# Performance work log

Measured on AMD Instinct MI355X. Metric: run time of the kernel, lower is better.

## Reference

```python
import jax, jax.numpy as jnp
import numpy as np

TOP_K = 2  # config.top_k


def setup_inputs() -> dict:
    key = jax.random.key(0)
    k0, k1, k2, k3, k4 = jax.random.split(key, 5)
    B, S, D, F, E = 1, 2048, 512, 1024, 8
    scale = 0.02
    hidden_states = jax.random.normal(k0, (B, S, D), dtype=jnp.float32)
    router_w = jax.random.normal(k1, (D, E), dtype=jnp.float32) * scale
    w1 = jax.random.normal(k2, (E, D, F), dtype=jnp.float32) * scale  # gate proj
    w2 = jax.random.normal(k3, (E, F, D), dtype=jnp.float32) * scale  # down proj
    w3 = jax.random.normal(k4, (E, D, F), dtype=jnp.float32) * scale  # up proj
    return {"hidden_states": hidden_states, "router_w": router_w,
            "w1": w1, "w2": w2, "w3": w3}


def reference(hidden_states, router_w, w1, w2, w3):
    B, S, D = hidden_states.shape
    E = router_w.shape[1]
    x = hidden_states.reshape(-1, D)                      # [T, D]
    T = x.shape[0]

    # router: softmax in float32, top-k, renormalize (matches torch source)
    router_logits = x @ router_w                          # [T, E]
    probs = jax.nn.softmax(router_logits.astype(jnp.float32), axis=-1)
    routing_weights, selected_experts = jax.lax.top_k(probs, TOP_K)  # [T, K]
    routing_weights = routing_weights / routing_weights.sum(axis=-1, keepdims=True)
    routing_weights = routing_weights.astype(x.dtype)

    # combine weights: scatter top-k weights into dense [T, E] (one-hot combine)
    combine = jnp.zeros((T, E), dtype=x.dtype).at[
        jnp.arange(T)[:, None], selected_experts].add(routing_weights)

    # dense-all-experts evaluation, math-identical to gather-GEMM-scatter:
    # unselected experts get combine weight 0 and contribute nothing.
    gate = jax.nn.silu(jnp.einsum('td,edf->tef', x, w1))  # [T, E, F]
    up = jnp.einsum('td,edf->tef', x, w3)                 # [T, E, F]
    h = gate * up * combine[:, :, None]                   # weight before down-proj
    out = jnp.einsum('tef,efd->td', h, w2)                # [T, D]
    return out.reshape(B, S, D)
```

## Files before the change

kernel.cpp:

```cpp
#include <hip/hip_runtime.h>
#include <hip/hip_bf16.h>


typedef __attribute__((ext_vector_type(4))) float f32x4;
typedef __attribute__((ext_vector_type(8))) __bf16 bf16x8;

#define T_TOK 2048
#define DMODEL 512
#define FFN 1024
#define NE 8
#define MAXMB 40
#define PCAP (MAXMB * 128)

__device__ __forceinline__ void gload_lds16(const void* g, void* l) {
  __builtin_amdgcn_global_load_lds(
      (const __attribute__((address_space(1))) void*)g,
      (__attribute__((address_space(3))) void*)l, 16, 0, 0);
}

#define PIPE_BAR_8()                                        \
  asm volatile("s_waitcnt vmcnt(8)" ::: "memory");          \
  __builtin_amdgcn_s_barrier();                             \
  __builtin_amdgcn_sched_barrier(0)
#define PIPE_BAR_6()                                        \
  asm volatile("s_waitcnt vmcnt(6)" ::: "memory");          \
  __builtin_amdgcn_s_barrier();                             \
  __builtin_amdgcn_sched_barrier(0)
#define PIPE_BAR_0()                                        \
  asm volatile("s_waitcnt vmcnt(0)" ::: "memory");          \
  __builtin_amdgcn_s_barrier();                             \
  __builtin_amdgcn_sched_barrier(0)
#define POST_BAR()                                          \
  __builtin_amdgcn_s_barrier();                             \
  __builtin_amdgcn_sched_barrier(0)

__global__ __launch_bounds__(256) void prep_kernel(
    const float* __restrict__ x, const float* __restrict__ rw,
    const float* __restrict__ w1, const float* __restrict__ w2,
    const float* __restrict__ w3, __bf16* __restrict__ xb,
    __bf16* __restrict__ w1t, __bf16* __restrict__ w2t,
    __bf16* __restrict__ w3t, int* __restrict__ tope, float* __restrict__ topw,
    int* __restrict__ pair_t, float* __restrict__ pair_w,
    int* __restrict__ sched_e) {
  __shared__ __bf16 tile[64][65];
  const int bx = blockIdx.x;
  const int tid = threadIdx.x;

  if (bx < 3072) {
    const float* src;
    __bf16* dst;
    int R, C, idx;
    if (bx < 1024)      { src = w1; dst = w1t; R = 512;  C = 1024; idx = bx; }
    else if (bx < 2048) { src = w3; dst = w3t; R = 512;  C = 1024; idx = bx - 1024; }
    else                { src = w2; dst = w2t; R = 1024; C = 512;  idx = bx - 2048; }
    const int ntx = C >> 6, nty = R >> 6;
    const int cx = idx % ntx;
    const int gry = idx / ntx;
    const int e = gry / nty;
    const int r0 = (gry % nty) * 64;
    const int c0 = cx * 64;
    src += (size_t)e * R * C;
    dst += (size_t)e * R * C;
#pragma unroll
    for (int q = 0; q < 4; ++q) {
      const int r = (tid >> 4) + q * 16;
      const int c = (tid & 15) * 4;
      const f32x4 v = *(const f32x4*)&src[(size_t)(r0 + r) * C + c0 + c];
      tile[r][c] = (__bf16)v[0];
      tile[r][c + 1] = (__bf16)v[1];
      tile[r][c + 2] = (__bf16)v[2];
      tile[r][c + 3] = (__bf16)v[3];
    }
    __syncthreads();
#pragma unroll
    for (int p = 0; p < 2; ++p) {
      const int cc = (tid >> 3) + p * 32;
      const int rr = (tid & 7) * 8;
      union { bf16x8 v; __bf16 s[8]; } u;
#pragma unroll
      for (int i = 0; i < 8; ++i) u.s[i] = tile[rr + i][cc];
      *(bf16x8*)&dst[(size_t)(c0 + cc) * R + r0 + rr] = u.v;
    }
  } else if (bx < 3584) {
    const int t = (bx - 3072) * 4 + (tid >> 6);
    const int lane = tid & 63;
    const float* xr = x + (size_t)t * DMODEL + lane * 8;
    const f32x4 a = *(const f32x4*)xr;
    const f32x4 b = *(const f32x4*)(xr + 4);
    bf16x8 v;
    v[0] = (__bf16)a[0]; v[1] = (__bf16)a[1]; v[2] = (__bf16)a[2]; v[3] = (__bf16)a[3];
    v[4] = (__bf16)b[0]; v[5] = (__bf16)b[1]; v[6] = (__bf16)b[2]; v[7] = (__bf16)b[3];
    *(bf16x8*)&xb[(size_t)t * DMODEL + lane * 8] = v;

    float xv[8] = {a[0], a[1], a[2], a[3], b[0], b[1], b[2], b[3]};
    float part[NE];
#pragma unroll
    for (int e = 0; e < NE; ++e) part[e] = 0.f;
#pragma unroll
    for (int i = 0; i < 8; ++i) {
      const int d = lane * 8 + i;
      const f32x4 r0 = *(const f32x4*)&rw[(size_t)d * NE];
      const f32x4 r1 = *(const f32x4*)&rw[(size_t)d * NE + 4];
      part[0] += xv[i] * r0[0]; part[1] += xv[i] * r0[1];
      part[2] += xv[i] * r0[2]; part[3] += xv[i] * r0[3];
      part[4] += xv[i] * r1[0]; part[5] += xv[i] * r1[1];
      part[6] += xv[i] * r1[2]; part[7] += xv[i] * r1[3];
    }
#pragma unroll
    for (int off = 32; off > 0; off >>= 1) {
#pragma unroll
      for (int e = 0; e < NE; ++e) part[e] += __shfl_xor(part[e], off);
    }
    if (lane == 0) {
      int ia = 0;
#pragma unroll
      for (int e = 1; e < NE; ++e)
        if (part[e] > part[ia]) ia = e;
      int ib = (ia == 0) ? 1 : 0;
#pragma unroll
      for (int e = 0; e < NE; ++e)
        if (e != ia && e != ib && part[e] > part[ib]) ib = e;
      const float wa = 1.f / (1.f + __expf(part[ib] - part[ia]));
      tope[t * 2] = ia;
      tope[t * 2 + 1] = ib;
      topw[t * 2] = wa;
      topw[t * 2 + 1] = 1.f - wa;
    }
  } else {
    const int i = (bx - 3584) * 256 + tid;
    for (int j = i; j < PCAP; j += 2048) { pair_t[j] = 0; pair_w[j] = 0.f; }
    if (i < MAXMB) sched_e[i] = -1;
  }
}

__global__ __launch_bounds__(256) void build_kernel(
    const int* __restrict__ tope, const float* __restrict__ topw,
    int* __restrict__ pair_t, float* __restrict__ pair_w,
    int* __restrict__ pairidx, int* __restrict__ sched_e) {
  __shared__ int cnt[NE], base[NE], ofs[NE];
  const int tid = threadIdx.x;
  if (tid < NE) { cnt[tid] = 0; ofs[tid] = 0; }
  __syncthreads();
  for (int t = tid; t < T_TOK; t += 256) {
    atomicAdd(&cnt[tope[t * 2]], 1);
    atomicAdd(&cnt[tope[t * 2 + 1]], 1);
  }
  __syncthreads();
  if (tid == 0) {
    int mb = 0;
    for (int e = 0; e < NE; ++e) {
      base[e] = mb * 128;
      const int nmb = (cnt[e] + 127) >> 7;
      for (int i = 0; i < nmb; ++i) sched_e[mb + i] = e;
      mb += nmb;
    }
  }
  __syncthreads();
  for (int t = tid; t < T_TOK; t += 256) {
#pragma unroll
    for (int s = 0; s < 2; ++s) {
      const int e = tope[t * 2 + s];
      const int pos = base[e] + atomicAdd(&ofs[e], 1);
      pair_t[pos] = t;
      pair_w[pos] = topw[t * 2 + s];
      pairidx[t * 2 + s] = pos;
    }
  }
}

__global__ __launch_bounds__(256) void gemm1_kernel(
    const __bf16* __restrict__ xb, const __bf16* __restrict__ w1t,
    const __bf16* __restrict__ w3t, const int* __restrict__ pair_t,
    const float* __restrict__ pair_w, const int* __restrict__ sched_e,
    __bf16* __restrict__ hbuf) {
  __shared__ alignas(16) __bf16 As[2][128 * 64];
  __shared__ alignas(16) __bf16 B1s[2][64 * 64];
  __shared__ alignas(16) __bf16 B3s[2][64 * 64];
  __shared__ float comb[128];
  const int tid = threadIdx.x;
  const int id = blockIdx.x;
  const int mb = (id & 7) + ((id >> 7) << 3);
  const int f0 = ((id >> 3) & 15) * 64;
  const int e = sched_e[mb];
  if (e < 0) return;
  const int m0 = mb * 128;
  const int lane = tid & 63;
  const int wv = tid >> 6;
  const int wr = wv >> 1, wc = wv & 1;
  const int l15 = lane & 15, lhi = lane >> 4;
  const int sw = (l15 & 7) << 4;

  if (tid < 128) comb[tid] = pair_w[m0 + tid];

  size_t aoff[4];
  int lbA[4];
#pragma unroll
  for (int it = 0; it < 4; ++it) {
    const int chunk = it * 256 + tid;
    const int r = chunk >> 3;
    const int c8 = ((chunk & 7) ^ (r & 7)) * 8;
    aoff[it] = (size_t)pair_t[m0 + r] * DMODEL + c8;
    lbA[it] = (it * 256 + (tid & ~63)) * 16;
  }
  size_t boff[2];
  int lbB[2];
#pragma unroll
  for (int it = 0; it < 2; ++it) {
    const int chunk = it * 256 + tid;
    const int r = chunk >> 3;
    const int c8 = ((chunk & 7) ^ (r & 7)) * 8;
    boff[it] = (size_t)(e * FFN + f0 + r) * DMODEL + c8;
    lbB[it] = (it * 256 + (tid & ~63)) * 16;
  }

  const f32x4 fz = {0.f, 0.f, 0.f, 0.f};
  f32x4 acc1[4][2], acc3[4][2];
#pragma unroll
  for (int m = 0; m < 4; ++m)
#pragma unroll
    for (int n = 0; n < 2; ++n) { acc1[m][n] = fz; acc3[m][n] = fz; }

#define G1_STAGE(BUF, K0)                                                     \
  do {                                                                        \
    _Pragma("unroll") for (int it = 0; it < 4; ++it)                          \
        gload_lds16(xb + aoff[it] + (K0), (char*)As[BUF] + lbA[it]);          \
    _Pragma("unroll") for (int it = 0; it < 2; ++it) {                        \
      gload_lds16(w1t + boff[it] + (K0), (char*)B1s[BUF] + lbB[it]);          \
      gload_lds16(w3t + boff[it] + (K0), (char*)B3s[BUF] + lbB[it]);          \
    }                                                                         \
  } while (0)

#define G1_COMPUTE(BUF)                                                       \
  do {                                                                        \
    __builtin_amdgcn_s_setprio(1);                                            \
    _Pragma("unroll") for (int kk = 0; kk < 2; ++kk) {                        \
      const int ko = (kk * 64 + lhi * 16) ^ sw;                               \
      bf16x8 af[4], b1f[2], b3f[2];                                           \
      _Pragma("unroll") for (int m = 0; m < 4; ++m)                           \
          af[m] = *(const bf16x8*)((const char*)As[BUF] +                     \
                                   (wr * 64 + m * 16 + l15) * 128 + ko);      \
      _Pragma("unroll") for (int n = 0; n < 2; ++n) {                         \
        const int ro = (wc * 32 + n * 16 + l15) * 128 + ko;                   \
        b1f[n] = *(const bf16x8*)((const char*)B1s[BUF] + ro);                \
        b3f[n] = *(const bf16x8*)((const char*)B3s[BUF] + ro);                \
      }                                                                       \
      _Pragma("unroll") for (int m = 0; m < 4; ++m)                           \
          _Pragma("unroll") for (int n = 0; n < 2; ++n) {                     \
        acc1[m][n] = __builtin_amdgcn_mfma_f32_16x16x32_bf16(af[m], b1f[n],   \
                                                             acc1[m][n], 0, 0, 0); \
        acc3[m][n] = __builtin_amdgcn_mfma_f32_16x16x32_bf16(af[m], b3f[n],   \
                                                             acc3[m][n], 0, 0, 0); \
      }                                                                       \
    }                                                                         \
    __builtin_amdgcn_s_setprio(0);                                            \
  } while (0)

  G1_STAGE(0, 0);
#pragma unroll
  for (int t = 0; t < 7; ++t) {
    G1_STAGE((t + 1) & 1, (t + 1) * 64);
    PIPE_BAR_8();
    G1_COMPUTE(t & 1);
    POST_BAR();
  }
  PIPE_BAR_0();
  G1_COMPUTE(1);

  __syncthreads();
  {
    __bf16* eps = (__bf16*)As;
    constexpr int EW = 72;
#pragma unroll
    for (int m = 0; m < 4; ++m)
#pragma unroll
      for (int n = 0; n < 2; ++n)
#pragma unroll
        for (int r = 0; r < 4; ++r) {
          const int row = wr * 64 + m * 16 + lhi * 4 + r;
          const int col = wc * 32 + n * 16 + l15;
          const float g = acc1[m][n][r];
          const float u = acc3[m][n][r];
          eps[row * EW + col] = (__bf16)((g / (1.f + __expf(-g))) * u * comb[row]);
        }
    __syncthreads();
#pragma unroll
    for (int p = 0; p < 4; ++p) {
      const int i = p * 256 + tid;
      const int row = i >> 3, c8 = (i & 7) * 8;
      *(bf16x8*)&hbuf[(size_t)(m0 + row) * FFN + f0 + c8] =
          *(const bf16x8*)&eps[row * EW + c8];
    }
  }
#undef G1_STAGE
#undef G1_COMPUTE
}

__global__ __launch_bounds__(256) void gemm2_kernel(
    const __bf16* __restrict__ hbuf, const __bf16* __restrict__ w2t,
    const int* __restrict__ sched_e, __bf16* __restrict__ outp) {
  __shared__ alignas(16) __bf16 As[2][128 * 64];
  __shared__ alignas(16) __bf16 Bs[2][64 * 64];
  const int tid = threadIdx.x;
  const int id = blockIdx.x;
  const int gk = (id & 7) + ((id >> 6) << 3);
  const int n0 = ((id >> 3) & 7) * 64;
  const int mb = gk >> 1;
  const int kz = gk & 1;
  const int e = sched_e[mb];
  if (e < 0) return;
  const int m0 = mb * 128;
  const int fbase = kz * (FFN / 2);
  const int lane = tid & 63;
  const int wv = tid >> 6;
  const int wr = wv >> 1, wc = wv & 1;
  const int l15 = lane & 15, lhi = lane >> 4;
  const int sw = (l15 & 7) << 4;

  size_t aoff[4];
  int lbA[4];
#pragma unroll
  for (int it = 0; it < 4; ++it) {
    const int chunk = it * 256 + tid;
    const int r = chunk >> 3;
    const int c8 = ((chunk & 7) ^ (r & 7)) * 8;
    aoff[it] = (size_t)(m0 + r) * FFN + fbase + c8;
    lbA[it] = (it * 256 + (tid & ~63)) * 16;
  }
  size_t boff[2];
  int lbB[2];
#pragma unroll
  for (int it = 0; it < 2; ++it) {
    const int chunk = it * 256 + tid;
    const int r = chunk >> 3;
    const int c8 = ((chunk & 7) ^ (r & 7)) * 8;
    boff[it] = ((size_t)e * DMODEL + n0 + r) * FFN + fbase + c8;
    lbB[it] = (it * 256 + (tid & ~63)) * 16;
  }

  const f32x4 fz = {0.f, 0.f, 0.f, 0.f};
  f32x4 acc[4][2];
#pragma unroll
  for (int m = 0; m < 4; ++m) { acc[m][0] = fz; acc[m][1] = fz; }

#define G2_STAGE(BUF, K0)                                                     \
  do {                                                                        \
    _Pragma("unroll") for (int it = 0; it < 4; ++it)                          \
        gload_lds16(hbuf + aoff[it] + (K0), (char*)As[BUF] + lbA[it]);        \
    _Pragma("unroll") for (int it = 0; it < 2; ++it)                          \
        gload_lds16(w2t + boff[it] + (K0), (char*)Bs[BUF] + lbB[it]);         \
  } while (0)

#define G2_COMPUTE(BUF)                                                       \
  do {                                                                        \
    __builtin_amdgcn_s_setprio(1);                                            \
    _Pragma("unroll") for (int kk = 0; kk < 2; ++kk) {                        \
      const int ko = (kk * 64 + lhi * 16) ^ sw;                               \
      bf16x8 af[4], bfr[2];                                                   \
      _Pragma("unroll") for (int m = 0; m < 4; ++m)                           \
          af[m] = *(const bf16x8*)((const char*)As[BUF] +                     \
                                   (wr * 64 + m * 16 + l15) * 128 + ko);      \
      _Pragma("unroll") for (int n = 0; n < 2; ++n)                           \
          bfr[n] = *(const bf16x8*)((const char*)Bs[BUF] +                    \
                                    (wc * 32 + n * 16 + l15) * 128 + ko);     \
      _Pragma("unroll") for (int m = 0; m < 4; ++m)                           \
          _Pragma("unroll") for (int n = 0; n < 2; ++n)                       \
              acc[m][n] = __builtin_amdgcn_mfma_f32_16x16x32_bf16(            \
                  af[m], bfr[n], acc[m][n], 0, 0, 0);                         \
    }                                                                         \
    __builtin_amdgcn_s_setprio(0);                                            \
  } while (0)

  G2_STAGE(0, 0);
#pragma unroll
  for (int t = 0; t < 7; ++t) {
    G2_STAGE((t + 1) & 1, (t + 1) * 64);
    PIPE_BAR_6();
    G2_COMPUTE(t & 1);
    POST_BAR();
  }
  PIPE_BAR_0();
  G2_COMPUTE(1);

  __syncthreads();
  {
    __bf16* eps = (__bf16*)As;
    constexpr int EW = 72;
#pragma unroll
    for (int m = 0; m < 4; ++m)
#pragma unroll
      for (int n = 0; n < 2; ++n)
#pragma unroll
        for (int r = 0; r < 4; ++r) {
          const int row = wr * 64 + m * 16 + lhi * 4 + r;
          const int col = wc * 32 + n * 16 + l15;
          eps[row * EW + col] = (__bf16)acc[m][n][r];
        }
    __syncthreads();
#pragma unroll
    for (int p = 0; p < 4; ++p) {
      const int i = p * 256 + tid;
      const int row = i >> 3, c8 = (i & 7) * 8;
      *(bf16x8*)&outp[((size_t)kz * PCAP + m0 + row) * DMODEL + n0 + c8] =
          *(const bf16x8*)&eps[row * EW + c8];
    }
  }
#undef G2_STAGE
#undef G2_COMPUTE
}

__global__ __launch_bounds__(256) void gather_kernel(
    const __bf16* __restrict__ outp, const int* __restrict__ pairidx,
    float* __restrict__ out) {
  const int i = blockIdx.x * 256 + threadIdx.x;
  const int t = i >> 6;
  const int c = (i & 63) * 8;
  const int p0 = pairidx[t * 2];
  const int p1 = pairidx[t * 2 + 1];
  const size_t KZ = (size_t)PCAP * DMODEL;
  const bf16x8 a0 = *(const bf16x8*)&outp[(size_t)p0 * DMODEL + c];
  const bf16x8 a1 = *(const bf16x8*)&outp[(size_t)p1 * DMODEL + c];
  const bf16x8 b0 = *(const bf16x8*)&outp[KZ + (size_t)p0 * DMODEL + c];
  const bf16x8 b1 = *(const bf16x8*)&outp[KZ + (size_t)p1 * DMODEL + c];
  f32x4 lo, hi;
#pragma unroll
  for (int j = 0; j < 4; ++j)
    lo[j] = (float)a0[j] + (float)a1[j] + (float)b0[j] + (float)b1[j];
#pragma unroll
  for (int j = 0; j < 4; ++j)
    hi[j] = (float)a0[j + 4] + (float)a1[j + 4] + (float)b0[j + 4] + (float)b1[j + 4];
  float* op = out + (size_t)t * DMODEL + c;
  *(f32x4*)op = lo;
  *(f32x4*)(op + 4) = hi;
}

extern "C" void kernel_launch(void* const* d_in, const int* in_sizes, int n_in,
                              void* d_out, int out_size, void* d_ws, size_t ws_size,
                              hipStream_t stream) {
  const float* x = (const float*)d_in[0];
  const float* rw = (const float*)d_in[1];
  const float* w1 = (const float*)d_in[2];
  const float* w2 = (const float*)d_in[3];
  const float* w3 = (const float*)d_in[4];
  float* out = (float*)d_out;
  char* ws = (char*)d_ws;

  int* tope = (int*)(ws + 0);
  float* topw = (float*)(ws + 16384);
  int* pair_t = (int*)(ws + 32768);
  float* pair_w = (float*)(ws + 53248);
  int* pairidx = (int*)(ws + 73728);
  int* sched_e = (int*)(ws + 90112);
  __bf16* xb = (__bf16*)(ws + 98304);
  __bf16* w1t = (__bf16*)(ws + 2195456);
  __bf16* w3t = (__bf16*)(ws + 10584064);
  __bf16* w2t = (__bf16*)(ws + 18972672);
  __bf16* hbuf = (__bf16*)(ws + 27361280);
  __bf16* outp = (__bf16*)(ws + 37847040);

  hipLaunchKernelGGL(prep_kernel, dim3(3592), dim3(256), 0, stream,
                     x, rw, w1, w2, w3, xb, w1t, w2t, w3t, tope, topw,
                     pair_t, pair_w, sched_e);
  hipLaunchKernelGGL(build_kernel, dim3(1), dim3(256), 0, stream,
                     tope, topw, pair_t, pair_w, pairidx, sched_e);
  hipLaunchKernelGGL(gemm1_kernel, dim3(640), dim3(256), 0, stream,
                     xb, w1t, w3t, pair_t, pair_w, sched_e, hbuf);
  hipLaunchKernelGGL(gemm2_kernel, dim3(640), dim3(256), 0, stream,
                     hbuf, w2t, sched_e, outp);
  hipLaunchKernelGGL(gather_kernel, dim3(512), dim3(256), 0, stream,
                     outp, pairidx, out);
}
```

Baseline: 72.90 us.

## Fuse weight fp32-to-bf16 transpose into GEMM B-tile staging

Removes the separate weight transpose/convert pass from the prep kernel. The GEMM kernels now load fp32 weights straight into registers, convert them to bf16 and write them transposed and swizzled into LDS. This avoids writing and re-reading the bf16 weight copies (about 24 MB of extra traffic). In exchange, each M-block re-reads the fp32 weights, which are twice as wide, and the pipeline is reworked so that each stage waits on vmcnt(0) before the register-to-LDS write, which may reduce overlap.

```diff
diff --git a/kernel.cpp b/kernel.cpp
--- a/kernel.cpp
+++ b/kernel.cpp
@@ -4,6 +4,7 @@
 
 typedef __attribute__((ext_vector_type(4))) float f32x4;
 typedef __attribute__((ext_vector_type(8))) __bf16 bf16x8;
+typedef __attribute__((ext_vector_type(2))) __bf16 bf16x2;
 
 #define T_TOK 2048
 #define DMODEL 512
@@ -18,71 +19,23 @@
       (__attribute__((address_space(3))) void*)l, 16, 0, 0);
 }
 
-#define PIPE_BAR_8()                                        \
-  asm volatile("s_waitcnt vmcnt(8)" ::: "memory");          \
+#define VM0()                                               \
+  asm volatile("s_waitcnt vmcnt(0)" ::: "memory");          \
+  __builtin_amdgcn_sched_barrier(0)
+#define LG0_BAR()                                           \
+  asm volatile("s_waitcnt lgkmcnt(0)" ::: "memory");        \
   __builtin_amdgcn_s_barrier();                             \
   __builtin_amdgcn_sched_barrier(0)
-#define PIPE_BAR_6()                                        \
-  asm volatile("s_waitcnt vmcnt(6)" ::: "memory");          \
-  __builtin_amdgcn_s_barrier();                             \
-  __builtin_amdgcn_sched_barrier(0)
-#define PIPE_BAR_0()                                        \
-  asm volatile("s_waitcnt vmcnt(0)" ::: "memory");          \
-  __builtin_amdgcn_s_barrier();                             \
-  __builtin_amdgcn_sched_barrier(0)
-#define POST_BAR()                                          \
-  __builtin_amdgcn_s_barrier();                             \
-  __builtin_amdgcn_sched_barrier(0)
 
 __global__ __launch_bounds__(256) void prep_kernel(
     const float* __restrict__ x, const float* __restrict__ rw,
-    const float* __restrict__ w1, const float* __restrict__ w2,
-    const float* __restrict__ w3, __bf16* __restrict__ xb,
-    __bf16* __restrict__ w1t, __bf16* __restrict__ w2t,
-    __bf16* __restrict__ w3t, int* __restrict__ tope, float* __restrict__ topw,
+    __bf16* __restrict__ xb, int* __restrict__ tope, float* __restrict__ topw,
     int* __restrict__ pair_t, float* __restrict__ pair_w,
     int* __restrict__ sched_e) {
-  __shared__ __bf16 tile[64][65];
   const int bx = blockIdx.x;
   const int tid = threadIdx.x;
-
-  if (bx < 3072) {
-    const float* src;
-    __bf16* dst;
-    int R, C, idx;
-    if (bx < 1024)      { src = w1; dst = w1t; R = 512;  C = 1024; idx = bx; }
-    else if (bx < 2048) { src = w3; dst = w3t; R = 512;  C = 1024; idx = bx - 1024; }
-    else                { src = w2; dst = w2t; R = 1024; C = 512;  idx = bx - 2048; }
-    const int ntx = C >> 6, nty = R >> 6;
-    const int cx = idx % ntx;
-    const int gry = idx / ntx;
-    const int e = gry / nty;
-    const int r0 = (gry % nty) * 64;
-    const int c0 = cx * 64;
-    src += (size_t)e * R * C;
-    dst += (size_t)e * R * C;
-#pragma unroll
-    for (int q = 0; q < 4; ++q) {
-      const int r = (tid >> 4) + q * 16;
-      const int c = (tid & 15) * 4;
-      const f32x4 v = *(const f32x4*)&src[(size_t)(r0 + r) * C + c0 + c];
-      tile[r][c] = (__bf16)v[0];
-      tile[r][c + 1] = (__bf16)v[1];
-      tile[r][c + 2] = (__bf16)v[2];
-      tile[r][c + 3] = (__bf16)v[3];
-    }
-    __syncthreads();
-#pragma unroll
-    for (int p = 0; p < 2; ++p) {
-      const int cc = (tid >> 3) + p * 32;
-      const int rr = (tid & 7) * 8;
-      union { bf16x8 v; __bf16 s[8]; } u;
-#pragma unroll
-      for (int i = 0; i < 8; ++i) u.s[i] = tile[rr + i][cc];
-      *(bf16x8*)&dst[(size_t)(c0 + cc) * R + r0 + rr] = u.v;
-    }
-  } else if (bx < 3584) {
-    const int t = (bx - 3072) * 4 + (tid >> 6);
+  if (bx < 512) {
+    const int t = bx * 4 + (tid >> 6);
     const int lane = tid & 63;
     const float* xr = x + (size_t)t * DMODEL + lane * 8;
     const f32x4 a = *(const f32x4*)xr;
@@ -127,7 +80,7 @@
       topw[t * 2 + 1] = 1.f - wa;
     }
   } else {
-    const int i = (bx - 3584) * 256 + tid;
+    const int i = (bx - 512) * 256 + tid;
     for (int j = i; j < PCAP; j += 2048) { pair_t[j] = 0; pair_w[j] = 0.f; }
     if (i < MAXMB) sched_e[i] = -1;
   }
@@ -169,8 +122,8 @@
 }
 
 __global__ __launch_bounds__(256) void gemm1_kernel(
-    const __bf16* __restrict__ xb, const __bf16* __restrict__ w1t,
-    const __bf16* __restrict__ w3t, const int* __restrict__ pair_t,
+    const __bf16* __restrict__ xb, const float* __restrict__ w1,
+    const float* __restrict__ w3, const int* __restrict__ pair_t,
     const float* __restrict__ pair_w, const int* __restrict__ sched_e,
     __bf16* __restrict__ hbuf) {
   __shared__ alignas(16) __bf16 As[2][128 * 64];
@@ -189,6 +142,7 @@
   const int wr = wv >> 1, wc = wv & 1;
   const int l15 = lane & 15, lhi = lane >> 4;
   const int sw = (l15 & 7) << 4;
+  const int dp = tid & 31, fq = tid >> 5;
 
   if (tid < 128) comb[tid] = pair_w[m0 + tid];
 
@@ -202,16 +156,8 @@
     aoff[it] = (size_t)pair_t[m0 + r] * DMODEL + c8;
     lbA[it] = (it * 256 + (tid & ~63)) * 16;
   }
-  size_t boff[2];
-  int lbB[2];
-#pragma unroll
-  for (int it = 0; it < 2; ++it) {
-    const int chunk = it * 256 + tid;
-    const int r = chunk >> 3;
-    const int c8 = ((chunk & 7) ^ (r & 7)) * 8;
-    boff[it] = (size_t)(e * FFN + f0 + r) * DMODEL + c8;
-    lbB[it] = (it * 256 + (tid & ~63)) * 16;
-  }
+  const float* b1base = w1 + ((size_t)e * DMODEL + 2 * dp) * FFN + f0 + fq * 8;
+  const float* b3base = w3 + ((size_t)e * DMODEL + 2 * dp) * FFN + f0 + fq * 8;
 
   const f32x4 fz = {0.f, 0.f, 0.f, 0.f};
   f32x4 acc1[4][2], acc3[4][2];
@@ -220,13 +166,36 @@
 #pragma unroll
     for (int n = 0; n < 2; ++n) { acc1[m][n] = fz; acc3[m][n] = fz; }
 
-#define G1_STAGE(BUF, K0)                                                     \
+  f32x4 q1[4], q3[4];
+
+#define G1_LOADB(K0)                                                          \
+  do {                                                                        \
+    const float* p1 = b1base + (size_t)(K0)*FFN;                              \
+    const float* p3 = b3base + (size_t)(K0)*FFN;                              \
+    q1[0] = *(const f32x4*)p1;        q1[1] = *(const f32x4*)(p1 + 4);        \
+    q1[2] = *(const f32x4*)(p1 + FFN); q1[3] = *(const f32x4*)(p1 + FFN + 4); \
+    q3[0] = *(const f32x4*)p3;        q3[1] = *(const f32x4*)(p3 + 4);        \
+    q3[2] = *(const f32x4*)(p3 + FFN); q3[3] = *(const f32x4*)(p3 + FFN + 4); \
+  } while (0)
+
+#define G1_STAGEA(BUF, K0)                                                    \
   do {                                                                        \
     _Pragma("unroll") for (int it = 0; it < 4; ++it)                          \
         gload_lds16(xb + aoff[it] + (K0), (char*)As[BUF] + lbA[it]);          \
-    _Pragma("unroll") for (int it = 0; it < 2; ++it) {                        \
-      gload_lds16(w1t + boff[it] + (K0), (char*)B1s[BUF] + lbB[it]);          \
-      gload_lds16(w3t + boff[it] + (K0), (char*)B3s[BUF] + lbB[it]);          \
+  } while (0)
+
+#define G1_WRITEB(BUF)                                                        \
+  do {                                                                        \
+    _Pragma("unroll") for (int fi = 0; fi < 8; ++fi) {                        \
+      const float l1 = fi < 4 ? q1[0][fi] : q1[1][fi - 4];                    \
+      const float h1 = fi < 4 ? q1[2][fi] : q1[3][fi - 4];                    \
+      const float l3 = fi < 4 ? q3[0][fi] : q3[1][fi - 4];                    \
+      const float h3 = fi < 4 ? q3[2][fi] : q3[3][fi - 4];                    \
+      const int ad = (fq * 8 + fi) * 128 + ((dp * 4) ^ (fi << 4));            \
+      bf16x2 v1 = {(__bf16)l1, (__bf16)h1};                                   \
+      bf16x2 v3 = {(__bf16)l3, (__bf16)h3};                                   \
+      *(bf16x2*)((char*)B1s[BUF] + ad) = v1;                                  \
+      *(bf16x2*)((char*)B3s[BUF] + ad) = v3;                                  \
     }                                                                         \
   } while (0)
 
@@ -255,15 +224,20 @@
     __builtin_amdgcn_s_setprio(0);                                            \
   } while (0)
 
-  G1_STAGE(0, 0);
+  G1_LOADB(0);
+  G1_STAGEA(0, 0);
+  VM0();
+  G1_WRITEB(0);
+  LG0_BAR();
 #pragma unroll
   for (int t = 0; t < 7; ++t) {
-    G1_STAGE((t + 1) & 1, (t + 1) * 64);
-    PIPE_BAR_8();
+    G1_LOADB((t + 1) * 64);
+    G1_STAGEA((t + 1) & 1, (t + 1) * 64);
     G1_COMPUTE(t & 1);
-    POST_BAR();
-  }
-  PIPE_BAR_0();
+    VM0();
+    G1_WRITEB((t + 1) & 1);
+    LG0_BAR();
+  }
   G1_COMPUTE(1);
 
   __syncthreads();
@@ -291,12 +265,14 @@
           *(const bf16x8*)&eps[row * EW + c8];
     }
   }
-#undef G1_STAGE
+#undef G1_LOADB
+#undef G1_STAGEA
+#undef G1_WRITEB
 #undef G1_COMPUTE
 }
 
 __global__ __launch_bounds__(256) void gemm2_kernel(
-    const __bf16* __restrict__ hbuf, const __bf16* __restrict__ w2t,
+    const __bf16* __restrict__ hbuf, const float* __restrict__ w2,
     const int* __restrict__ sched_e, __bf16* __restrict__ outp) {
   __shared__ alignas(16) __bf16 As[2][128 * 64];
   __shared__ alignas(16) __bf16 Bs[2][64 * 64];
@@ -315,6 +291,7 @@
   const int wr = wv >> 1, wc = wv & 1;
   const int l15 = lane & 15, lhi = lane >> 4;
   const int sw = (l15 & 7) << 4;
+  const int fp = tid & 31, dq = tid >> 5;
 
   size_t aoff[4];
   int lbA[4];
@@ -326,28 +303,37 @@
     aoff[it] = (size_t)(m0 + r) * FFN + fbase + c8;
     lbA[it] = (it * 256 + (tid & ~63)) * 16;
   }
-  size_t boff[2];
-  int lbB[2];
-#pragma unroll
-  for (int it = 0; it < 2; ++it) {
-    const int chunk = it * 256 + tid;
-    const int r = chunk >> 3;
-    const int c8 = ((chunk & 7) ^ (r & 7)) * 8;
-    boff[it] = ((size_t)e * DMODEL + n0 + r) * FFN + fbase + c8;
-    lbB[it] = (it * 256 + (tid & ~63)) * 16;
-  }
+  const float* bbase = w2 + ((size_t)e * FFN + fbase + 2 * fp) * DMODEL + n0 + dq * 8;
 
   const f32x4 fz = {0.f, 0.f, 0.f, 0.f};
   f32x4 acc[4][2];
 #pragma unroll
   for (int m = 0; m < 4; ++m) { acc[m][0] = fz; acc[m][1] = fz; }
 
-#define G2_STAGE(BUF, K0)                                                     \
+  f32x4 q[4];
+
+#define G2_LOADB(K0)                                                          \
+  do {                                                                        \
+    const float* p = bbase + (size_t)(K0)*DMODEL;                             \
+    q[0] = *(const f32x4*)p;            q[1] = *(const f32x4*)(p + 4);        \
+    q[2] = *(const f32x4*)(p + DMODEL); q[3] = *(const f32x4*)(p + DMODEL + 4);\
+  } while (0)
+
+#define G2_STAGEA(BUF, K0)                                                    \
   do {                                                                        \
     _Pragma("unroll") for (int it = 0; it < 4; ++it)                          \
         gload_lds16(hbuf + aoff[it] + (K0), (char*)As[BUF] + lbA[it]);        \
-    _Pragma("unroll") for (int it = 0; it < 2; ++it)                          \
-        gload_lds16(w2t + boff[it] + (K0), (char*)Bs[BUF] + lbB[it]);         \
+  } while (0)
+
+#define G2_WRITEB(BUF)                                                        \
+  do {                                                                        \
+    _Pragma("unroll") for (int i = 0; i < 8; ++i) {                           \
+      const float lo = i < 4 ? q[0][i] : q[1][i - 4];                         \
+      const float hi = i < 4 ? q[2][i] : q[3][i - 4];                         \
+      const int ad = (dq * 8 + i) * 128 + ((fp * 4) ^ (i << 4));              \
+      bf16x2 v = {(__bf16)lo, (__bf16)hi};                                    \
+      *(bf16x2*)((char*)Bs[BUF] + ad) = v;                                    \
+    }                                                                         \
   } while (0)
 
 #define G2_COMPUTE(BUF)                                                       \
@@ -370,15 +356,20 @@
     __builtin_amdgcn_s_setprio(0);                                            \
   } while (0)
 
-  G2_STAGE(0, 0);
+  G2_LOADB(0);
+  G2_STAGEA(0, 0);
+  VM0();
+  G2_WRITEB(0);
+  LG0_BAR();
 #pragma unroll
   for (int t = 0; t < 7; ++t) {
-    G2_STAGE((t + 1) & 1, (t + 1) * 64);
-    PIPE_BAR_6();
+    G2_LOADB((t + 1) * 64);
+    G2_STAGEA((t + 1) & 1, (t + 1) * 64);
     G2_COMPUTE(t & 1);
-    POST_BAR();
-  }
-  PIPE_BAR_0();
+    VM0();
+    G2_WRITEB((t + 1) & 1);
+    LG0_BAR();
+  }
   G2_COMPUTE(1);
 
   __syncthreads();
@@ -404,7 +395,9 @@
           *(const bf16x8*)&eps[row * EW + c8];
     }
   }
-#undef G2_STAGE
+#undef G2_LOADB
+#undef G2_STAGEA
+#undef G2_WRITEB
 #undef G2_COMPUTE
 }
 
@@ -451,21 +444,17 @@
   int* pairidx = (int*)(ws + 73728);
   int* sched_e = (int*)(ws + 90112);
   __bf16* xb = (__bf16*)(ws + 98304);
-  __bf16* w1t = (__bf16*)(ws + 2195456);
-  __bf16* w3t = (__bf16*)(ws + 10584064);
-  __bf16* w2t = (__bf16*)(ws + 18972672);
-  __bf16* hbuf = (__bf16*)(ws + 27361280);
-  __bf16* outp = (__bf16*)(ws + 37847040);
-
-  hipLaunchKernelGGL(prep_kernel, dim3(3592), dim3(256), 0, stream,
-                     x, rw, w1, w2, w3, xb, w1t, w2t, w3t, tope, topw,
-                     pair_t, pair_w, sched_e);
+  __bf16* hbuf = (__bf16*)(ws + 2195456);
+  __bf16* outp = (__bf16*)(ws + 12681216);
+
+  hipLaunchKernelGGL(prep_kernel, dim3(520), dim3(256), 0, stream,
+                     x, rw, xb, tope, topw, pair_t, pair_w, sched_e);
   hipLaunchKernelGGL(build_kernel, dim3(1), dim3(256), 0, stream,
                      tope, topw, pair_t, pair_w, pairidx, sched_e);
   hipLaunchKernelGGL(gemm1_kernel, dim3(640), dim3(256), 0, stream,
-                     xb, w1t, w3t, pair_t, pair_w, sched_e, hbuf);
+                     xb, w1, w3, pair_t, pair_w, sched_e, hbuf);
   hipLaunchKernelGGL(gemm2_kernel, dim3(640), dim3(256), 0, stream,
-                     hbuf, w2t, sched_e, outp);
+                     hbuf, w2, sched_e, outp);
   hipLaunchKernelGGL(gather_kernel, dim3(512), dim3(256), 0, stream,
                      outp, pairidx, out);
 }
```

New measurement: 86.48 us. 1.19x slower.
